# Kernel tuning notes

Measured on AMD Instinct MI355X. Metric: run time of the kernel, lower is better.

## Reference

```python
import jax, jax.numpy as jnp
import numpy as np

B, T, D, H, E = 4, 2048, 1024, 4096, 8


def setup_inputs() -> dict:
    key = jax.random.key(0)
    ks = jax.random.split(key, 7)
    x = jax.random.normal(ks[0], (B, T, D), dtype=jnp.float32)
    # Gate: Linear(D, E)
    Wg = jax.random.normal(ks[1], (D, E), dtype=jnp.float32) / np.sqrt(D)
    bg = jax.random.normal(ks[2], (E,), dtype=jnp.float32) * 0.01
    # Experts: E x [Linear(D,H), ReLU, Linear(H,D)] (dropout inactive at eval)
    W1 = jax.random.normal(ks[3], (E, D, H), dtype=jnp.float32) / np.sqrt(D)
    b1 = jax.random.normal(ks[4], (E, H), dtype=jnp.float32) * 0.01
    W2 = jax.random.normal(ks[5], (E, H, D), dtype=jnp.float32) / np.sqrt(H)
    b2 = jax.random.normal(ks[6], (E, D), dtype=jnp.float32) * 0.01
    return {"x": x, "Wg": Wg, "bg": bg, "W1": W1, "b1": b1, "W2": W2, "b2": b2}


def reference(x, Wg, bg, W1, b1, W2, b2):
    # Gate + hard top-1 routing
    gate_scores = x @ Wg + bg                      # [B,T,E]
    top1 = jnp.argmax(gate_scores, axis=-1)        # [B,T]
    onehot = jax.nn.one_hot(top1, Wg.shape[-1], dtype=x.dtype)  # [B,T,E]
    # Dense: every expert MLP over all tokens (matches original's masked
    # formulation: x*mask == x on selected tokens, output re-masked).
    h = jax.nn.relu(jnp.einsum('btd,edh->beth', x, W1) + b1[None, :, None, :])
    y = jnp.einsum('beth,ehd->betd', h, W2) + b2[None, :, None, :]
    # Masked combine: keep only the token's chosen expert output
    out = jnp.einsum('betd,bte->btd', y, onehot)
    return out
```

## Files before the change

### kernel.cpp

```cpp
#include <hip/hip_runtime.h>
#include <hip/hip_bf16.h>
#include <stdint.h>

#define NTOK 8192
#define DDIM 1024
#define HDIM 4096
#define NEXP 8
#define MAXWL 48

typedef __attribute__((ext_vector_type(4))) float f32x4;
typedef __attribute__((ext_vector_type(8))) short s16x8;
typedef __attribute__((ext_vector_type(8))) unsigned short u16x8;

__device__ __forceinline__ unsigned short f2bf(float f) {
  union { float f; unsigned int u; } v; v.f = f;
  unsigned int u = v.u;
  u += 0x7FFFu + ((u >> 16) & 1u);
  return (unsigned short)(u >> 16);
}

typedef __attribute__((address_space(3))) unsigned char lds_u8;
typedef const __attribute__((address_space(1))) unsigned char glb_u8;

__device__ __forceinline__ void load_lds16(const void* g, void* l) {
  __builtin_amdgcn_global_load_lds((glb_u8*)g, (lds_u8*)l, 16, 0, 0);
}

template <int VM> __device__ __forceinline__ void wait_vm() {
  if constexpr (VM == 8) asm volatile("s_waitcnt vmcnt(8)" ::: "memory");
  else if constexpr (VM == 4) asm volatile("s_waitcnt vmcnt(4)" ::: "memory");
  else asm volatile("s_waitcnt vmcnt(0)" ::: "memory");
}

__global__ __launch_bounds__(256) void gate_kernel(
    const float* __restrict__ x, const float* __restrict__ Wg,
    const float* __restrict__ bg, int* __restrict__ counts,
    int* __restrict__ lists) {
  const int lane = threadIdx.x & 63;
  const int tok = blockIdx.x * 4 + (threadIdx.x >> 6);
  const float* xr = x + (size_t)tok * DDIM;
  double acc[NEXP];
#pragma unroll
  for (int e = 0; e < NEXP; ++e) acc[e] = 0.0;
#pragma unroll 4
  for (int it = 0; it < DDIM / 64; ++it) {
    const int d = it * 64 + lane;
    const float xv = xr[d];
    const f32x4 w0 = *(const f32x4*)(Wg + (size_t)d * NEXP);
    const f32x4 w1 = *(const f32x4*)(Wg + (size_t)d * NEXP + 4);
#pragma unroll
    for (int j = 0; j < 4; ++j) {
      acc[j]     += (double)xv * (double)w0[j];
      acc[4 + j] += (double)xv * (double)w1[j];
    }
  }
#pragma unroll
  for (int e = 0; e < NEXP; ++e) {
    double v = acc[e];
#pragma unroll
    for (int off = 32; off > 0; off >>= 1) v += __shfl_xor(v, off, 64);
    acc[e] = v;
  }
  if (lane == 0) {
    int best = 0;
    double bv = acc[0] + (double)bg[0];
#pragma unroll
    for (int e = 1; e < NEXP; ++e) {
      const double v = acc[e] + (double)bg[e];
      if (v > bv) { bv = v; best = e; }
    }
    const int pos = atomicAdd(&counts[best], 1);
    lists[best * NTOK + pos] = tok;
  }
}

__global__ void offs_kernel(const int* __restrict__ counts, int* __restrict__ offs,
                            int* __restrict__ wl) {
  int s = 0;
#pragma unroll
  for (int e = 0; e < NEXP; ++e) { offs[e] = s; s += counts[e]; }
  offs[NEXP] = s;
  int n = 0;
  for (int e = 0; e < NEXP; ++e) {
    const int nb = (counts[e] + 255) >> 8;
    for (int b = 0; b < nb; ++b) wl[n++] = (e << 20) | b;
  }
  offs[NEXP + 1] = n;
}

__global__ __launch_bounds__(256) void gather_conv_kernel(
    const float* __restrict__ x, const int* __restrict__ offs,
    const int* __restrict__ lists, int* __restrict__ stok,
    unsigned short* __restrict__ xbs) {
  const int p = blockIdx.x * 4 + (threadIdx.x >> 6);
  const int lane = threadIdx.x & 63;
  int e = 0;
#pragma unroll
  for (int k = 1; k < NEXP; ++k) e += (p >= offs[k]) ? 1 : 0;
  const int tok = lists[e * NTOK + (p - offs[e])];
  if (lane == 0) stok[p] = tok;
  const float* src = x + (size_t)tok * DDIM + lane * 16;
  unsigned short* dst = xbs + (size_t)p * DDIM + lane * 16;
#pragma unroll
  for (int q = 0; q < 2; ++q) {
    const f32x4 a = *(const f32x4*)(src + q * 8);
    const f32x4 b = *(const f32x4*)(src + q * 8 + 4);
    u16x8 o;
#pragma unroll
    for (int j = 0; j < 4; ++j) { o[j] = f2bf(a[j]); o[4 + j] = f2bf(b[j]); }
    *(u16x8*)(dst + q * 8) = o;
  }
}

__global__ __launch_bounds__(256) void transpose_conv_kernel(
    const float* __restrict__ in, unsigned short* __restrict__ out,
    int R, int C) {
  __shared__ unsigned short T[64][66];
  const int e = blockIdx.z;
  const float* ine = in + (size_t)e * R * C;
  unsigned short* oute = out + (size_t)e * C * R;
  const int c0 = blockIdx.x * 64, r0 = blockIdx.y * 64;
  const int t = threadIdx.x;
  const int tr = t >> 4, tc4 = (t & 15) * 4;
#pragma unroll
  for (int p = 0; p < 4; ++p) {
    const int r = tr + p * 16;
    const f32x4 v = *(const f32x4*)(ine + (size_t)(r0 + r) * C + c0 + tc4);
#pragma unroll
    for (int j = 0; j < 4; ++j) T[r][tc4 + j] = f2bf(v[j]);
  }
  __syncthreads();
#pragma unroll
  for (int p = 0; p < 4; ++p) {
    const int c = tr + p * 16;
    ushort4 o;
    o.x = T[tc4 + 0][c]; o.y = T[tc4 + 1][c];
    o.z = T[tc4 + 2][c]; o.w = T[tc4 + 3][c];
    *(ushort4*)(oute + (size_t)(c0 + c) * R + r0 + tc4) = o;
  }
}

template <int K, int N, int NCB, bool FUSE1>
__global__ __launch_bounds__(512, 2) void ffn_kernel(
    const unsigned short* __restrict__ A, const unsigned short* __restrict__ Bt,
    const float* __restrict__ bias, const int* __restrict__ counts,
    const int* __restrict__ offs, const int* __restrict__ wl,
    const int* __restrict__ stok, unsigned short* __restrict__ outb,
    float* __restrict__ outf) {
  constexpr int NT = K / 32;
  static_assert((NT & 3) == 0 && NT >= 8, "");
  constexpr int NWG = NCB * MAXWL;
  static_assert((NWG & 7) == 0, "");

  const int d = blockIdx.x;
  const int logical = (d & 7) * (NWG / 8) + (d >> 3);
  const int col0 = (logical / MAXWL) * 256;
  const int wli = logical % MAXWL;
  if (wli >= offs[NEXP + 1]) return;
  const int wle = wl[wli];
  const int e = wle >> 20;
  const int bx = wle & 0xFFFFF;
  const int cnt = counts[e];
  const int row0 = offs[e] + bx * 256;

  __shared__ __align__(16) unsigned short As0[256 * 32], Bs0[256 * 32];
  __shared__ __align__(16) unsigned short As1[256 * 32], Bs1[256 * 32];
  __shared__ __align__(16) unsigned short As2[256 * 32], Bs2[256 * 32];
  __shared__ __align__(16) unsigned short As3[256 * 32], Bs3[256 * 32];

  const int tid = threadIdx.x;
  const int lane = tid & 63;
  const int w = tid >> 6;
  const int wm = w >> 2;
  const int wn = w & 3;
  const int fr = lane & 15;
  const int fj = lane >> 4;

  const int swsrc = (((tid & 3) ^ ((tid >> 2) & 3) ^ ((tid >> 4) & 3))) * 8;
  int gr0 = row0 + (tid >> 2);        if (gr0 > NTOK - 1) gr0 = NTOK - 1;
  int gr1 = row0 + 128 + (tid >> 2);  if (gr1 > NTOK - 1) gr1 = NTOK - 1;
  const unsigned short* srcA0 = A + (size_t)gr0 * K + swsrc;
  const unsigned short* srcA1 = A + (size_t)gr1 * K + swsrc;
  const unsigned short* Bte = Bt + (size_t)e * N * K;
  const unsigned short* srcB0 = Bte + (size_t)(col0 + (tid >> 2)) * K + swsrc;
  const unsigned short* srcB1 = Bte + (size_t)(col0 + 128 + (tid >> 2)) * K + swsrc;

  const int js = ((fj ^ (fr & 3) ^ ((fr >> 2) & 3))) * 8;

  f32x4 acc[8][4];
#pragma unroll
  for (int m = 0; m < 8; ++m)
#pragma unroll
    for (int n = 0; n < 4; ++n) acc[m][n] = f32x4{0.f, 0.f, 0.f, 0.f};

  auto stage = [&](unsigned short* nA, unsigned short* nB, int kel) {
    load_lds16(srcA0 + kel, nA + tid * 8);
    load_lds16(srcA1 + kel, nA + 4096 + tid * 8);
    load_lds16(srcB0 + kel, nB + tid * 8);
    load_lds16(srcB1 + kel, nB + 4096 + tid * 8);
  };

  auto body = [&](const unsigned short* pA, const unsigned short* pB,
                  unsigned short* nA, unsigned short* nB, int knext,
                  bool do_stage) {
    __builtin_amdgcn_s_barrier();
    asm volatile("" ::: "memory");
    if (do_stage) stage(nA, nB, knext);
    s16x8 af[8], bf[4];
#pragma unroll
    for (int m = 0; m < 8; ++m)
      af[m] = *(const s16x8*)(pA + (wm * 128 + m * 16 + fr) * 32 + js);
#pragma unroll
    for (int n = 0; n < 4; ++n)
      bf[n] = *(const s16x8*)(pB + (wn * 64 + n * 16 + fr) * 32 + js);
    __builtin_amdgcn_s_setprio(1);
#pragma unroll
    for (int m = 0; m < 8; ++m)
#pragma unroll
      for (int n = 0; n < 4; ++n)
        acc[m][n] = __builtin_amdgcn_mfma_f32_16x16x32_bf16(af[m], bf[n],
                                                            acc[m][n], 0, 0, 0);
    __builtin_amdgcn_s_setprio(0);
  };

  stage(As0, Bs0, 0);
  stage(As1, Bs1, 32);
  stage(As2, Bs2, 64);

#pragma unroll 1
  for (int t = 0; t < NT - 4; t += 4) {
    wait_vm<8>(); body(As0, Bs0, As3, Bs3, (t + 3) * 32, true);
    wait_vm<8>(); body(As1, Bs1, As0, Bs0, (t + 4) * 32, true);
    wait_vm<8>(); body(As2, Bs2, As1, Bs1, (t + 5) * 32, true);
    wait_vm<8>(); body(As3, Bs3, As2, Bs2, (t + 6) * 32, true);
  }
  wait_vm<8>(); body(As0, Bs0, As3, Bs3, (NT - 1) * 32, true);
  wait_vm<8>(); body(As1, Bs1, nullptr, nullptr, 0, false);
  wait_vm<4>(); body(As2, Bs2, nullptr, nullptr, 0, false);
  wait_vm<0>(); body(As3, Bs3, nullptr, nullptr, 0, false);

#pragma unroll
  for (int n = 0; n < 4; ++n) {
    const int col = col0 + wn * 64 + n * 16 + fr;
    const float bv = bias[e * N + col];
#pragma unroll
    for (int m = 0; m < 8; ++m) {
#pragma unroll
      for (int j = 0; j < 4; ++j) {
        const int rl = wm * 128 + m * 16 + fj * 4 + j;
        if (bx * 256 + rl < cnt) {
          if constexpr (FUSE1) {
            outb[(size_t)(row0 + rl) * N + col] = f2bf(fmaxf(acc[m][n][j] + bv, 0.f));
          } else {
            outf[(size_t)stok[row0 + rl] * N + col] = acc[m][n][j] + bv;
          }
        }
      }
    }
  }
}

extern "C" void kernel_launch(void* const* d_in, const int* in_sizes, int n_in,
                              void* d_out, int out_size, void* d_ws, size_t ws_size,
                              hipStream_t stream) {
  (void)in_sizes; (void)n_in; (void)out_size;
  const float* x  = (const float*)d_in[0];
  const float* Wg = (const float*)d_in[1];
  const float* bg = (const float*)d_in[2];
  const float* W1 = (const float*)d_in[3];
  const float* b1 = (const float*)d_in[4];
  const float* W2 = (const float*)d_in[5];
  const float* b2 = (const float*)d_in[6];
  float* out = (float*)d_out;

  char* ws = (char*)d_ws;
  const size_t OFF_CNT = 0;
  const size_t OFF_OFF = 128;
  const size_t OFF_WL  = 256;
  const size_t OFF_LST = 1024;
  const size_t OFF_STK = OFF_LST + (size_t)NEXP * NTOK * 4;
  const size_t OFF_XBS = OFF_STK + (size_t)NTOK * 4;
  const size_t OFF_HS  = OFF_XBS + (size_t)NTOK * DDIM * 2;
  const size_t OFF_WT  = OFF_HS + (size_t)NTOK * HDIM * 2;
  const size_t NEED    = OFF_WT + (size_t)NEXP * DDIM * HDIM * 2;
  if (ws_size < NEED) return;

  int* counts = (int*)(ws + OFF_CNT);
  int* offs   = (int*)(ws + OFF_OFF);
  int* wl     = (int*)(ws + OFF_WL);
  int* lists  = (int*)(ws + OFF_LST);
  int* stok   = (int*)(ws + OFF_STK);
  unsigned short* xbs = (unsigned short*)(ws + OFF_XBS);
  unsigned short* Hs  = (unsigned short*)(ws + OFF_HS);
  unsigned short* Wt  = (unsigned short*)(ws + OFF_WT);

  hipMemsetAsync(counts, 0, 128, stream);
  gate_kernel<<<NTOK / 4, 256, 0, stream>>>(x, Wg, bg, counts, lists);
  offs_kernel<<<1, 1, 0, stream>>>(counts, offs, wl);
  gather_conv_kernel<<<NTOK / 4, 256, 0, stream>>>(x, offs, lists, stok, xbs);

  transpose_conv_kernel<<<dim3(HDIM / 64, DDIM / 64, NEXP), 256, 0, stream>>>(
      W1, Wt, DDIM, HDIM);
  ffn_kernel<DDIM, HDIM, HDIM / 256, true>
      <<<dim3((HDIM / 256) * MAXWL), 512, 0, stream>>>(
          xbs, Wt, b1, counts, offs, wl, stok, Hs, nullptr);
  transpose_conv_kernel<<<dim3(DDIM / 64, HDIM / 64, NEXP), 256, 0, stream>>>(
      W2, Wt, HDIM, DDIM);
  ffn_kernel<HDIM, DDIM, DDIM / 256, false>
      <<<dim3((DDIM / 256) * MAXWL), 512, 0, stream>>>(
          Hs, Wt, b2, counts, offs, wl, stok, nullptr, out);
}
```

Baseline: 469.7 us.

## Narrow second FFN GEMM tile to 128 columns and simplify LDS swizzle

The FFN GEMM kernel is templated on tile width BN, and the second GEMM (N=1024) now uses 128-column tiles. This doubles the number of workgroups so more CUs stay busy on the small-N GEMM, at the cost of less reuse of the A tile. The vmcnt waits are scaled to the reduced B load count. The LDS swizzle pattern is changed, and the transpose kernel now writes 16-byte vectors instead of 8-byte ones to cut store instructions.

```diff
diff --git a/kernel.cpp b/kernel.cpp
--- a/kernel.cpp
+++ b/kernel.cpp
@@ -27,9 +27,11 @@
 }
 
 template <int VM> __device__ __forceinline__ void wait_vm() {
-  if constexpr (VM == 8) asm volatile("s_waitcnt vmcnt(8)" ::: "memory");
+  if constexpr (VM == 8)      asm volatile("s_waitcnt vmcnt(8)" ::: "memory");
+  else if constexpr (VM == 6) asm volatile("s_waitcnt vmcnt(6)" ::: "memory");
   else if constexpr (VM == 4) asm volatile("s_waitcnt vmcnt(4)" ::: "memory");
-  else asm volatile("s_waitcnt vmcnt(0)" ::: "memory");
+  else if constexpr (VM == 3) asm volatile("s_waitcnt vmcnt(3)" ::: "memory");
+  else                        asm volatile("s_waitcnt vmcnt(0)" ::: "memory");
 }
 
 __global__ __launch_bounds__(256) void gate_kernel(
@@ -130,43 +132,48 @@
     for (int j = 0; j < 4; ++j) T[r][tc4 + j] = f2bf(v[j]);
   }
   __syncthreads();
-#pragma unroll
-  for (int p = 0; p < 4; ++p) {
-    const int c = tr + p * 16;
-    ushort4 o;
-    o.x = T[tc4 + 0][c]; o.y = T[tc4 + 1][c];
-    o.z = T[tc4 + 2][c]; o.w = T[tc4 + 3][c];
-    *(ushort4*)(oute + (size_t)(c0 + c) * R + r0 + tc4) = o;
-  }
-}
-
-template <int K, int N, int NCB, bool FUSE1>
+  const int cc = t >> 3, rr8 = (t & 7) * 8;
+#pragma unroll
+  for (int p = 0; p < 2; ++p) {
+    const int c = cc + p * 32;
+    u16x8 o;
+#pragma unroll
+    for (int j = 0; j < 8; ++j) o[j] = T[rr8 + j][c];
+    *(u16x8*)(oute + (size_t)(c0 + c) * R + r0 + rr8) = o;
+  }
+}
+
+template <int BN, int K, int N, bool FUSE1>
 __global__ __launch_bounds__(512, 2) void ffn_kernel(
     const unsigned short* __restrict__ A, const unsigned short* __restrict__ Bt,
     const float* __restrict__ bias, const int* __restrict__ counts,
     const int* __restrict__ offs, const int* __restrict__ wl,
     const int* __restrict__ stok, unsigned short* __restrict__ outb,
     float* __restrict__ outf) {
+  constexpr int BM = 256;
+  constexpr int ISS_B = BN / 128;
+  constexpr int S = 2 + ISS_B;
+  constexpr int NF = BN / 64;
   constexpr int NT = K / 32;
-  static_assert((NT & 3) == 0 && NT >= 8, "");
+  constexpr int NCB = N / BN;
   constexpr int NWG = NCB * MAXWL;
-  static_assert((NWG & 7) == 0, "");
+  static_assert((NWG & 7) == 0 && (NT & 3) == 0 && NT >= 8, "");
 
   const int d = blockIdx.x;
   const int logical = (d & 7) * (NWG / 8) + (d >> 3);
-  const int col0 = (logical / MAXWL) * 256;
+  const int col0 = (logical / MAXWL) * BN;
   const int wli = logical % MAXWL;
   if (wli >= offs[NEXP + 1]) return;
   const int wle = wl[wli];
   const int e = wle >> 20;
   const int bx = wle & 0xFFFFF;
   const int cnt = counts[e];
-  const int row0 = offs[e] + bx * 256;
-
-  __shared__ __align__(16) unsigned short As0[256 * 32], Bs0[256 * 32];
-  __shared__ __align__(16) unsigned short As1[256 * 32], Bs1[256 * 32];
-  __shared__ __align__(16) unsigned short As2[256 * 32], Bs2[256 * 32];
-  __shared__ __align__(16) unsigned short As3[256 * 32], Bs3[256 * 32];
+  const int row0 = offs[e] + bx * BM;
+
+  __shared__ __align__(16) unsigned short As0[BM * 32], Bs0[BN * 32];
+  __shared__ __align__(16) unsigned short As1[BM * 32], Bs1[BN * 32];
+  __shared__ __align__(16) unsigned short As2[BM * 32], Bs2[BN * 32];
+  __shared__ __align__(16) unsigned short As3[BM * 32], Bs3[BN * 32];
 
   const int tid = threadIdx.x;
   const int lane = tid & 63;
@@ -176,28 +183,29 @@
   const int fr = lane & 15;
   const int fj = lane >> 4;
 
-  const int swsrc = (((tid & 3) ^ ((tid >> 2) & 3) ^ ((tid >> 4) & 3))) * 8;
-  int gr0 = row0 + (tid >> 2);        if (gr0 > NTOK - 1) gr0 = NTOK - 1;
-  int gr1 = row0 + 128 + (tid >> 2);  if (gr1 > NTOK - 1) gr1 = NTOK - 1;
+  const int swsrc = ((tid & 3) ^ ((tid >> 3) & 3)) * 8;
+  const int rb = tid >> 2;
+  int gr0 = row0 + rb;        if (gr0 > NTOK - 1) gr0 = NTOK - 1;
+  int gr1 = row0 + 128 + rb;  if (gr1 > NTOK - 1) gr1 = NTOK - 1;
   const unsigned short* srcA0 = A + (size_t)gr0 * K + swsrc;
   const unsigned short* srcA1 = A + (size_t)gr1 * K + swsrc;
   const unsigned short* Bte = Bt + (size_t)e * N * K;
-  const unsigned short* srcB0 = Bte + (size_t)(col0 + (tid >> 2)) * K + swsrc;
-  const unsigned short* srcB1 = Bte + (size_t)(col0 + 128 + (tid >> 2)) * K + swsrc;
-
-  const int js = ((fj ^ (fr & 3) ^ ((fr >> 2) & 3))) * 8;
-
-  f32x4 acc[8][4];
+  const unsigned short* srcB0 = Bte + (size_t)(col0 + rb) * K + swsrc;
+  const unsigned short* srcB1 = Bte + (size_t)(col0 + 128 + rb) * K + swsrc;
+
+  const int js = (fj ^ ((fr >> 1) & 3)) * 8;
+
+  f32x4 acc[8][NF];
 #pragma unroll
   for (int m = 0; m < 8; ++m)
 #pragma unroll
-    for (int n = 0; n < 4; ++n) acc[m][n] = f32x4{0.f, 0.f, 0.f, 0.f};
+    for (int n = 0; n < NF; ++n) acc[m][n] = f32x4{0.f, 0.f, 0.f, 0.f};
 
   auto stage = [&](unsigned short* nA, unsigned short* nB, int kel) {
     load_lds16(srcA0 + kel, nA + tid * 8);
     load_lds16(srcA1 + kel, nA + 4096 + tid * 8);
     load_lds16(srcB0 + kel, nB + tid * 8);
-    load_lds16(srcB1 + kel, nB + 4096 + tid * 8);
+    if constexpr (ISS_B == 2) load_lds16(srcB1 + kel, nB + 4096 + tid * 8);
   };
 
   auto body = [&](const unsigned short* pA, const unsigned short* pB,
@@ -206,18 +214,18 @@
     __builtin_amdgcn_s_barrier();
     asm volatile("" ::: "memory");
     if (do_stage) stage(nA, nB, knext);
-    s16x8 af[8], bf[4];
+    s16x8 af[8], bf[NF];
 #pragma unroll
     for (int m = 0; m < 8; ++m)
       af[m] = *(const s16x8*)(pA + (wm * 128 + m * 16 + fr) * 32 + js);
 #pragma unroll
-    for (int n = 0; n < 4; ++n)
-      bf[n] = *(const s16x8*)(pB + (wn * 64 + n * 16 + fr) * 32 + js);
+    for (int n = 0; n < NF; ++n)
+      bf[n] = *(const s16x8*)(pB + (wn * NF * 16 + n * 16 + fr) * 32 + js);
     __builtin_amdgcn_s_setprio(1);
 #pragma unroll
     for (int m = 0; m < 8; ++m)
 #pragma unroll
-      for (int n = 0; n < 4; ++n)
+      for (int n = 0; n < NF; ++n)
         acc[m][n] = __builtin_amdgcn_mfma_f32_16x16x32_bf16(af[m], bf[n],
                                                             acc[m][n], 0, 0, 0);
     __builtin_amdgcn_s_setprio(0);
@@ -229,26 +237,26 @@
 
 #pragma unroll 1
   for (int t = 0; t < NT - 4; t += 4) {
-    wait_vm<8>(); body(As0, Bs0, As3, Bs3, (t + 3) * 32, true);
-    wait_vm<8>(); body(As1, Bs1, As0, Bs0, (t + 4) * 32, true);
-    wait_vm<8>(); body(As2, Bs2, As1, Bs1, (t + 5) * 32, true);
-    wait_vm<8>(); body(As3, Bs3, As2, Bs2, (t + 6) * 32, true);
-  }
-  wait_vm<8>(); body(As0, Bs0, As3, Bs3, (NT - 1) * 32, true);
-  wait_vm<8>(); body(As1, Bs1, nullptr, nullptr, 0, false);
-  wait_vm<4>(); body(As2, Bs2, nullptr, nullptr, 0, false);
-  wait_vm<0>(); body(As3, Bs3, nullptr, nullptr, 0, false);
-
-#pragma unroll
-  for (int n = 0; n < 4; ++n) {
-    const int col = col0 + wn * 64 + n * 16 + fr;
+    wait_vm<2 * S>(); body(As0, Bs0, As3, Bs3, (t + 3) * 32, true);
+    wait_vm<2 * S>(); body(As1, Bs1, As0, Bs0, (t + 4) * 32, true);
+    wait_vm<2 * S>(); body(As2, Bs2, As1, Bs1, (t + 5) * 32, true);
+    wait_vm<2 * S>(); body(As3, Bs3, As2, Bs2, (t + 6) * 32, true);
+  }
+  wait_vm<2 * S>(); body(As0, Bs0, As3, Bs3, (NT - 1) * 32, true);
+  wait_vm<2 * S>(); body(As1, Bs1, nullptr, nullptr, 0, false);
+  wait_vm<S>();     body(As2, Bs2, nullptr, nullptr, 0, false);
+  wait_vm<0>();     body(As3, Bs3, nullptr, nullptr, 0, false);
+
+#pragma unroll
+  for (int n = 0; n < NF; ++n) {
+    const int col = col0 + wn * NF * 16 + n * 16 + fr;
     const float bv = bias[e * N + col];
 #pragma unroll
     for (int m = 0; m < 8; ++m) {
 #pragma unroll
       for (int j = 0; j < 4; ++j) {
         const int rl = wm * 128 + m * 16 + fj * 4 + j;
-        if (bx * 256 + rl < cnt) {
+        if (bx * BM + rl < cnt) {
           if constexpr (FUSE1) {
             outb[(size_t)(row0 + rl) * N + col] = f2bf(fmaxf(acc[m][n][j] + bv, 0.f));
           } else {
@@ -301,12 +309,12 @@
 
   transpose_conv_kernel<<<dim3(HDIM / 64, DDIM / 64, NEXP), 256, 0, stream>>>(
       W1, Wt, DDIM, HDIM);
-  ffn_kernel<DDIM, HDIM, HDIM / 256, true>
+  ffn_kernel<256, DDIM, HDIM, true>
       <<<dim3((HDIM / 256) * MAXWL), 512, 0, stream>>>(
           xbs, Wt, b1, counts, offs, wl, stok, Hs, nullptr);
   transpose_conv_kernel<<<dim3(DDIM / 64, HDIM / 64, NEXP), 256, 0, stream>>>(
       W2, Wt, HDIM, DDIM);
-  ffn_kernel<HDIM, DDIM, DDIM / 256, false>
-      <<<dim3((DDIM / 256) * MAXWL), 512, 0, stream>>>(
+  ffn_kernel<128, HDIM, DDIM, false>
+      <<<dim3((DDIM / 128) * MAXWL), 512, 0, stream>>>(
           Hs, Wt, b2, counts, offs, wl, stok, nullptr, out);
 }
```

Result: slower. 509.6 us (+8.5%).
